# Kernel tuning notes

Measured on AMD Instinct MI355X. Metric: run time of the kernel, lower is better.

Reference implementation:

```python
import jax, jax.numpy as jnp
import numpy as np

B, S, D = 2, 2048, 1024
H = 16
DH = D // H  # 64


def setup_inputs() -> dict:
    key = jax.random.key(0)
    ks = jax.random.split(key, 5)
    scale = 0.02
    x = jax.random.normal(ks[0], (B, S, D), dtype=jnp.float32)
    W_qkv = jax.random.normal(ks[1], (D, 3 * D), dtype=jnp.float32) * scale
    b_qkv = jnp.zeros((3 * D,), dtype=jnp.float32)
    W_out = jax.random.normal(ks[2], (D, D), dtype=jnp.float32) * scale
    b_out = jnp.zeros((D,), dtype=jnp.float32)
    return {"x": x, "W_qkv": W_qkv, "b_qkv": b_qkv, "W_out": W_out, "b_out": b_out}


def reference(x, W_qkv, b_qkv, W_out, b_out):
    # Fused QKV projection: [B,S,D] @ [D,3D] -> [B,S,3D]
    qkv = jnp.einsum('bsd,df->bsf', x, W_qkv) + b_qkv
    q, k, v = qkv[:, :, :D], qkv[:, :, D:2 * D], qkv[:, :, 2 * D:]
    # Split heads: [B,S,D] -> [B,H,S,DH]
    def split(t):
        return t.reshape(B, S, H, DH).transpose(0, 2, 1, 3)
    q, k, v = split(q), split(k), split(v)
    # Scaled dot-product attention (naive, full score matrix as in source)
    scores = jnp.einsum('bhqd,bhkd->bhqk', q, k) / jnp.sqrt(jnp.float32(DH))
    probs = jax.nn.softmax(scores, axis=-1)  # mask=None, dropout eval-mode identity
    attn = jnp.einsum('bhqk,bhkd->bhqd', probs, v)
    # Merge heads: [B,H,S,DH] -> [B,S,D]
    attn = attn.transpose(0, 2, 1, 3).reshape(B, S, D)
    out = jnp.einsum('bsd,de->bse', attn, W_out) + b_out
    return out
```

## Files before the change

kernel.cpp:

```cpp
#include <hip/hip_runtime.h>

typedef _Float16 half8  __attribute__((ext_vector_type(8)));
typedef _Float16 half4  __attribute__((ext_vector_type(4)));
typedef float    floatx4  __attribute__((ext_vector_type(4)));
typedef float    floatx16 __attribute__((ext_vector_type(16)));

constexpr int B_ = 2, S_ = 2048, D_ = 1024, H_ = 16, M_ = 4096;
constexpr float QSCALE = 0.18033688011112042f;

__device__ __forceinline__ void gload16(const void* g, void* l) {
  __builtin_amdgcn_global_load_lds((const __attribute__((address_space(1))) void*)g,
                                   (__attribute__((address_space(3))) void*)l, 16, 0, 0);
}

__global__ __launch_bounds__(256) void cast_f32_f16(const float* __restrict__ in,
                                                    _Float16* __restrict__ out, int n8) {
  int i = blockIdx.x * 256 + threadIdx.x;
  if (i >= n8) return;
  float4 a = reinterpret_cast<const float4*>(in)[2 * i];
  float4 b = reinterpret_cast<const float4*>(in)[2 * i + 1];
  half8 h;
  h[0] = (_Float16)a.x; h[1] = (_Float16)a.y; h[2] = (_Float16)a.z; h[3] = (_Float16)a.w;
  h[4] = (_Float16)b.x; h[5] = (_Float16)b.y; h[6] = (_Float16)b.z; h[7] = (_Float16)b.w;
  reinterpret_cast<half8*>(out)[i] = h;
}

__global__ __launch_bounds__(256) void transpose_cast(const float* __restrict__ W,
                                                      _Float16* __restrict__ WT,
                                                      int K, int N) {
  __shared__ float Ws[64][65];
  const int n0 = blockIdx.x * 64, k0 = blockIdx.y * 64;
  const int t = threadIdx.x;
#pragma unroll
  for (int i = 0; i < 4; i++) {
    int idx = t + 256 * i;
    int r = idx >> 4, c4 = idx & 15;
    float4 v = *reinterpret_cast<const float4*>(W + (size_t)(k0 + r) * N + n0 + c4 * 4);
    Ws[r][c4 * 4 + 0] = v.x; Ws[r][c4 * 4 + 1] = v.y;
    Ws[r][c4 * 4 + 2] = v.z; Ws[r][c4 * 4 + 3] = v.w;
  }
  __syncthreads();
#pragma unroll
  for (int i = 0; i < 2; i++) {
    int idx = t + 256 * i;
    int r = idx >> 3, ck = idx & 7;
    half8 h;
#pragma unroll
    for (int j = 0; j < 8; j++) h[j] = (_Float16)Ws[ck * 8 + j][r];
    *reinterpret_cast<half8*>(WT + (size_t)(n0 + r) * K + k0 + ck * 8) = h;
  }
}

template <bool OUT_HALF>
__global__ __launch_bounds__(256) void gemm_mfma(const _Float16* __restrict__ A,
                                                 const _Float16* __restrict__ BT,
                                                 const float* __restrict__ bias,
                                                 void* __restrict__ Cout,
                                                 int M, int N, int K,
                                                 float scale_lo, int ncut) {
  __shared__ _Float16 As[128 * 64];
  __shared__ _Float16 Bs[128 * 64];
  const int t = threadIdx.x, w = t >> 6, lane = t & 63;
  const int m0 = blockIdx.y * 128, n0 = blockIdx.x * 128;
  const int wr = (w >> 1) * 64, wc = (w & 1) * 64;

  floatx4 acc[4][4] = {};

  for (int k0 = 0; k0 < K; k0 += 64) {
    __syncthreads();
#pragma unroll
    for (int i = 0; i < 4; i++) {
      int idx = t + 256 * i;
      int r = idx >> 3, c = idx & 7;
      int cs = c ^ (r & 7);
      gload16(A + (size_t)(m0 + r) * K + k0 + cs * 8, (char*)As + idx * 16);
      gload16(BT + (size_t)(n0 + r) * K + k0 + cs * 8, (char*)Bs + idx * 16);
    }
    __syncthreads();
#pragma unroll
    for (int ks = 0; ks < 2; ks++) {
      half8 af[4], bf[4];
#pragma unroll
      for (int r = 0; r < 4; r++) {
        int row = wr + r * 16 + (lane & 15);
        int ch = (ks * 4 + (lane >> 4)) ^ (row & 7);
        af[r] = *reinterpret_cast<const half8*>((const char*)As + row * 128 + ch * 16);
      }
#pragma unroll
      for (int c = 0; c < 4; c++) {
        int row = wc + c * 16 + (lane & 15);
        int ch = (ks * 4 + (lane >> 4)) ^ (row & 7);
        bf[c] = *reinterpret_cast<const half8*>((const char*)Bs + row * 128 + ch * 16);
      }
#pragma unroll
      for (int r = 0; r < 4; r++)
#pragma unroll
        for (int c = 0; c < 4; c++)
          acc[r][c] = __builtin_amdgcn_mfma_f32_16x16x32_f16(af[r], bf[c], acc[r][c], 0, 0, 0);
    }
  }

#pragma unroll
  for (int r = 0; r < 4; r++)
#pragma unroll
    for (int c = 0; c < 4; c++) {
      int col = n0 + wc + c * 16 + (lane & 15);
      float bv = bias[col];
      float sc = (col < ncut) ? scale_lo : 1.0f;
#pragma unroll
      for (int reg = 0; reg < 4; reg++) {
        int row = m0 + wr + r * 16 + (lane >> 4) * 4 + reg;
        float v = (acc[r][c][reg] + bv) * sc;
        if (OUT_HALF)
          reinterpret_cast<_Float16*>(Cout)[(size_t)row * N + col] = (_Float16)v;
        else
          reinterpret_cast<float*>(Cout)[(size_t)row * N + col] = v;
      }
    }
}

__global__ __launch_bounds__(256) void v_transpose(const _Float16* __restrict__ qkv,
                                                   _Float16* __restrict__ Vt) {
  __shared__ _Float16 Vs[64][72];
  const int s0 = blockIdx.x * 64, bh = blockIdx.y;
  const int b = bh >> 4, h = bh & 15;
  const int t = threadIdx.x;
#pragma unroll
  for (int i = 0; i < 2; i++) {
    int idx = t + 256 * i;
    int r = idx >> 3, c = idx & 7;
    half8 v = *reinterpret_cast<const half8*>(
        qkv + (size_t)(b * S_ + s0 + r) * (3 * D_) + 2 * D_ + h * 64 + c * 8);
    *reinterpret_cast<half8*>(&Vs[r][c * 8]) = v;
  }
  __syncthreads();
#pragma unroll
  for (int i = 0; i < 2; i++) {
    int idx = t + 256 * i;
    int d = idx >> 3, c = idx & 7;
    half8 o;
#pragma unroll
    for (int j = 0; j < 8; j++) o[j] = Vs[c * 8 + j][d];
    *reinterpret_cast<half8*>(Vt + ((size_t)bh * 64 + d) * S_ + s0 + c * 8) = o;
  }
}

__global__ __launch_bounds__(256) void flash_mfma(const _Float16* __restrict__ qkv,
                                                  const _Float16* __restrict__ Vt,
                                                  _Float16* __restrict__ attn_out) {
  const int qt = blockIdx.x, h = blockIdx.y, b = blockIdx.z;
  const int t = threadIdx.x, w = t >> 6, lane = t & 63;
  const int lo = lane & 31, hi = lane >> 5;

  __shared__ _Float16 Ks[64 * 64];
  __shared__ _Float16 Vts[64 * 64];
  __shared__ _Float16 Ps[4 * 2048];

  const int qrow = qt * 128 + w * 32 + lo;
  const _Float16* qbase = qkv + (size_t)(b * S_ + qrow) * (3 * D_) + h * 64;
  half8 qf[4];
#pragma unroll
  for (int kd = 0; kd < 4; kd++)
    qf[kd] = *reinterpret_cast<const half8*>(qbase + kd * 16 + hi * 8);

  floatx16 s0, s1, o0, o1;
#pragma unroll
  for (int r = 0; r < 16; r++) { o0[r] = 0.f; o1[r] = 0.f; }
  float m = -1e30f, l = 0.f;

  const size_t kbase = (size_t)(b * S_) * (3 * D_) + D_ + h * 64;
  const size_t vbase = (size_t)(b * H_ + h) * 64 * S_;

  for (int kv0 = 0; kv0 < S_; kv0 += 64) {
    __syncthreads();
#pragma unroll
    for (int i = 0; i < 2; i++) {
      int idx = t + 256 * i;
      int r = idx >> 3, c = idx & 7, cs = c ^ (r & 7);
      gload16(qkv + kbase + (size_t)(kv0 + r) * (3 * D_) + cs * 8, (char*)Ks + idx * 16);
      gload16(Vt + vbase + (size_t)r * S_ + kv0 + cs * 8, (char*)Vts + idx * 16);
    }
    __syncthreads();

#pragma unroll
    for (int r = 0; r < 16; r++) { s0[r] = 0.f; s1[r] = 0.f; }
#pragma unroll
    for (int kd = 0; kd < 4; kd++) {
      int r0 = lo, r1 = 32 + lo;
      int ch = kd * 2 + hi;
      half8 k0f = *reinterpret_cast<const half8*>((const char*)Ks + r0 * 128 + ((ch ^ (r0 & 7)) * 16));
      half8 k1f = *reinterpret_cast<const half8*>((const char*)Ks + r1 * 128 + ((ch ^ (r1 & 7)) * 16));
      s0 = __builtin_amdgcn_mfma_f32_32x32x16_f16(k0f, qf[kd], s0, 0, 0, 0);
      s1 = __builtin_amdgcn_mfma_f32_32x32x16_f16(k1f, qf[kd], s1, 0, 0, 0);
    }

    float pm = -1e30f;
#pragma unroll
    for (int r = 0; r < 16; r++) pm = fmaxf(pm, fmaxf(s0[r], s1[r]));
    pm = fmaxf(pm, __shfl_xor(pm, 32));
    float mn = fmaxf(m, pm);
    float alpha = __builtin_amdgcn_exp2f(m - mn);
    m = mn;
    float rs = 0.f;
#pragma unroll
    for (int r = 0; r < 16; r++) {
      s0[r] = __builtin_amdgcn_exp2f(s0[r] - mn);
      s1[r] = __builtin_amdgcn_exp2f(s1[r] - mn);
      rs += s0[r] + s1[r];
    }
    rs += __shfl_xor(rs, 32);
    l = l * alpha + rs;
#pragma unroll
    for (int r = 0; r < 16; r++) { o0[r] *= alpha; o1[r] *= alpha; }

#pragma unroll
    for (int mt = 0; mt < 2; mt++)
#pragma unroll
      for (int rq = 0; rq < 4; rq++) {
        half4 pv;
#pragma unroll
        for (int e = 0; e < 4; e++) pv[e] = (_Float16)((mt ? s1 : s0)[4 * rq + e]);
        int ch = (4 * mt + rq) ^ (lo & 7);
        *reinterpret_cast<half4*>((char*)Ps + w * 4096 + lo * 128 + ch * 16 + hi * 8) = pv;
      }

#pragma unroll
    for (int ks = 0; ks < 4; ks++) {
      int ch = ks * 2 + hi;
      half8 pf = *reinterpret_cast<const half8*>(
          (const char*)Ps + w * 4096 + lo * 128 + ((ch ^ (lo & 7)) * 16));
      int r0 = lo, r1 = 32 + lo;
      half8 vf0 = *reinterpret_cast<const half8*>((const char*)Vts + r0 * 128 + ((ch ^ (r0 & 7)) * 16));
      half8 vf1 = *reinterpret_cast<const half8*>((const char*)Vts + r1 * 128 + ((ch ^ (r1 & 7)) * 16));
      o0 = __builtin_amdgcn_mfma_f32_32x32x16_f16(vf0, pf, o0, 0, 0, 0);
      o1 = __builtin_amdgcn_mfma_f32_32x32x16_f16(vf1, pf, o1, 0, 0, 0);
    }
  }

  float inv = 1.0f / l;
  _Float16* ob = attn_out + (size_t)(b * S_ + qt * 128 + w * 32 + lo) * D_ + h * 64;
#pragma unroll
  for (int mt = 0; mt < 2; mt++)
#pragma unroll
    for (int rq = 0; rq < 4; rq++) {
      half4 v;
#pragma unroll
      for (int e = 0; e < 4; e++) v[e] = (_Float16)((mt ? o1 : o0)[4 * rq + e] * inv);
      *reinterpret_cast<half4*>(ob + 32 * mt + 8 * rq + 4 * hi) = v;
    }
}

extern "C" void kernel_launch(void* const* d_in, const int* in_sizes, int n_in,
                              void* d_out, int out_size, void* d_ws, size_t ws_size,
                              hipStream_t stream) {
  const float* x     = (const float*)d_in[0];
  const float* W_qkv = (const float*)d_in[1];
  const float* b_qkv = (const float*)d_in[2];
  const float* W_out = (const float*)d_in[3];
  const float* b_out = (const float*)d_in[4];
  float* out = (float*)d_out;

  _Float16* xh   = (_Float16*)d_ws;
  _Float16* WqT  = xh   + (size_t)M_ * D_;
  _Float16* WoT  = WqT  + (size_t)3 * D_ * D_;
  _Float16* qkvh = WoT  + (size_t)D_ * D_;
  _Float16* Vth  = qkvh + (size_t)M_ * 3 * D_;
  _Float16* atth = Vth  + (size_t)B_ * H_ * 64 * S_;

  cast_f32_f16<<<(M_ * D_ / 8 + 255) / 256, 256, 0, stream>>>(x, xh, M_ * D_ / 8);
  transpose_cast<<<dim3(3 * D_ / 64, D_ / 64), 256, 0, stream>>>(W_qkv, WqT, D_, 3 * D_);
  transpose_cast<<<dim3(D_ / 64, D_ / 64), 256, 0, stream>>>(W_out, WoT, D_, D_);

  gemm_mfma<true><<<dim3(3 * D_ / 128, M_ / 128), 256, 0, stream>>>(
      xh, WqT, b_qkv, qkvh, M_, 3 * D_, D_, QSCALE, D_);

  v_transpose<<<dim3(S_ / 64, B_ * H_), 256, 0, stream>>>(qkvh, Vth);

  flash_mfma<<<dim3(S_ / 128, H_, B_), 256, 0, stream>>>(qkvh, Vth, atth);

  gemm_mfma<false><<<dim3(D_ / 128, M_ / 128), 256, 0, stream>>>(
      atth, WoT, b_out, out, M_, D_, D_, 1.0f, 0);
}
```

Baseline: 151.5 us.

## Double-buffer 128-wide KV tiles and keep P in registers via permlane swap

Restructures the flash attention loop to process 128-key tiles with double-buffered K/V shared memory, prefetching the next tile with async global-to-LDS loads while the current one computes. The LDS round-trip for the probability matrix is removed: P is packed to fp16 in registers and rearranged with v_permlane32_swap to form the MFMA operand directly. It also adds a lazy rescale that skips the output rescaling when the running max grows by no more than a threshold. The costs are more LDS and register pressure, and one wasted prefetch of a wrapped tile on the last iteration.

```diff
diff --git a/kernel.cpp b/kernel.cpp
--- a/kernel.cpp
+++ b/kernel.cpp
@@ -4,9 +4,11 @@
 typedef _Float16 half4  __attribute__((ext_vector_type(4)));
 typedef float    floatx4  __attribute__((ext_vector_type(4)));
 typedef float    floatx16 __attribute__((ext_vector_type(16)));
+typedef unsigned int uint4v __attribute__((ext_vector_type(4)));
 
 constexpr int B_ = 2, S_ = 2048, D_ = 1024, H_ = 16, M_ = 4096;
 constexpr float QSCALE = 0.18033688011112042f;
+constexpr int KVB = 128, NTILES = S_ / KVB;
 
 __device__ __forceinline__ void gload16(const void* g, void* l) {
   __builtin_amdgcn_global_load_lds((const __attribute__((address_space(1))) void*)g,
@@ -152,9 +154,8 @@
   const int t = threadIdx.x, w = t >> 6, lane = t & 63;
   const int lo = lane & 31, hi = lane >> 5;
 
-  __shared__ _Float16 Ks[64 * 64];
-  __shared__ _Float16 Vts[64 * 64];
-  __shared__ _Float16 Ps[4 * 2048];
+  __shared__ _Float16 Ks[2][KVB * 64];
+  __shared__ _Float16 Vts[2][64 * KVB];
 
   const int qrow = qt * 128 + w * 32 + lo;
   const _Float16* qbase = qkv + (size_t)(b * S_ + qrow) * (3 * D_) + h * 64;
@@ -162,90 +163,120 @@
 #pragma unroll
   for (int kd = 0; kd < 4; kd++)
     qf[kd] = *reinterpret_cast<const half8*>(qbase + kd * 16 + hi * 8);
-
-  floatx16 s0, s1, o0, o1;
+  asm volatile("" : "+v"(qf[0]), "+v"(qf[1]), "+v"(qf[2]), "+v"(qf[3]));
+
+  const size_t kbase = (size_t)(b * S_) * (3 * D_) + D_ + h * 64;
+  const size_t vbase = (size_t)(b * H_ + h) * 64 * S_;
+
+  auto stage = [&](int buf, int tile) {
+    const int kv0 = tile * KVB;
+    const _Float16* kg = qkv + kbase + (size_t)kv0 * (3 * D_);
+#pragma unroll
+    for (int p = 0; p < 4; p++) {
+      int idx = t + 256 * p;
+      int r = idx >> 3, c = idx & 7, cs = c ^ (r & 7);
+      gload16(kg + (size_t)r * (3 * D_) + cs * 8, (char*)&Ks[buf][0] + idx * 16);
+    }
+    const _Float16* vg = Vt + vbase + kv0;
+#pragma unroll
+    for (int p = 0; p < 4; p++) {
+      int idx = t + 256 * p;
+      int r = idx >> 4, c = idx & 15, cs = c ^ (r & 15);
+      gload16(vg + (size_t)r * S_ + cs * 8, (char*)&Vts[buf][0] + idx * 16);
+    }
+  };
+
+  floatx16 o0, o1;
 #pragma unroll
   for (int r = 0; r < 16; r++) { o0[r] = 0.f; o1[r] = 0.f; }
   float m = -1e30f, l = 0.f;
 
-  const size_t kbase = (size_t)(b * S_) * (3 * D_) + D_ + h * 64;
-  const size_t vbase = (size_t)(b * H_ + h) * 64 * S_;
-
-  for (int kv0 = 0; kv0 < S_; kv0 += 64) {
-    __syncthreads();
-#pragma unroll
-    for (int i = 0; i < 2; i++) {
-      int idx = t + 256 * i;
-      int r = idx >> 3, c = idx & 7, cs = c ^ (r & 7);
-      gload16(qkv + kbase + (size_t)(kv0 + r) * (3 * D_) + cs * 8, (char*)Ks + idx * 16);
-      gload16(Vt + vbase + (size_t)r * S_ + kv0 + cs * 8, (char*)Vts + idx * 16);
-    }
-    __syncthreads();
-
-#pragma unroll
-    for (int r = 0; r < 16; r++) { s0[r] = 0.f; s1[r] = 0.f; }
+  stage(0, 0);
+
+  for (int tt = 0; tt < NTILES; ++tt) {
+    const int cb = tt & 1;
+    stage(cb ^ 1, (tt + 1) & (NTILES - 1));
+    asm volatile("s_waitcnt vmcnt(8)" ::: "memory");
+    __builtin_amdgcn_s_barrier();
+    __builtin_amdgcn_sched_barrier(0);
+
+    const char* kb2 = (const char*)&Ks[cb][0];
+    floatx16 s[4];
+#pragma unroll
+    for (int sb = 0; sb < 4; sb++)
+#pragma unroll
+      for (int r = 0; r < 16; r++) s[sb][r] = 0.f;
 #pragma unroll
     for (int kd = 0; kd < 4; kd++) {
-      int r0 = lo, r1 = 32 + lo;
-      int ch = kd * 2 + hi;
-      half8 k0f = *reinterpret_cast<const half8*>((const char*)Ks + r0 * 128 + ((ch ^ (r0 & 7)) * 16));
-      half8 k1f = *reinterpret_cast<const half8*>((const char*)Ks + r1 * 128 + ((ch ^ (r1 & 7)) * 16));
-      s0 = __builtin_amdgcn_mfma_f32_32x32x16_f16(k0f, qf[kd], s0, 0, 0, 0);
-      s1 = __builtin_amdgcn_mfma_f32_32x32x16_f16(k1f, qf[kd], s1, 0, 0, 0);
+#pragma unroll
+      for (int sb = 0; sb < 4; sb++) {
+        int rr = sb * 32 + lo;
+        half8 kf = *reinterpret_cast<const half8*>(
+            kb2 + rr * 128 + (((kd * 2 + hi) ^ (rr & 7)) * 16));
+        s[sb] = __builtin_amdgcn_mfma_f32_32x32x16_f16(kf, qf[kd], s[sb], 0, 0, 0);
+      }
     }
 
     float pm = -1e30f;
 #pragma unroll
-    for (int r = 0; r < 16; r++) pm = fmaxf(pm, fmaxf(s0[r], s1[r]));
+    for (int sb = 0; sb < 4; sb++)
+#pragma unroll
+      for (int r = 0; r < 16; r++) pm = fmaxf(pm, s[sb][r]);
     pm = fmaxf(pm, __shfl_xor(pm, 32));
-    float mn = fmaxf(m, pm);
-    float alpha = __builtin_amdgcn_exp2f(m - mn);
-    m = mn;
+    if (!__all(pm <= m + 8.0f)) {
+      float mn = fmaxf(m, pm);
+      float al = __builtin_amdgcn_exp2f(m - mn);
+      m = mn; l *= al;
+#pragma unroll
+      for (int r = 0; r < 16; r++) { o0[r] *= al; o1[r] *= al; }
+    }
     float rs = 0.f;
 #pragma unroll
-    for (int r = 0; r < 16; r++) {
-      s0[r] = __builtin_amdgcn_exp2f(s0[r] - mn);
-      s1[r] = __builtin_amdgcn_exp2f(s1[r] - mn);
-      rs += s0[r] + s1[r];
-    }
+    for (int sb = 0; sb < 4; sb++)
+#pragma unroll
+      for (int r = 0; r < 16; r++) {
+        s[sb][r] = __builtin_amdgcn_exp2f(s[sb][r] - m);
+        rs += s[sb][r];
+      }
     rs += __shfl_xor(rs, 32);
-    l = l * alpha + rs;
-#pragma unroll
-    for (int r = 0; r < 16; r++) { o0[r] *= alpha; o1[r] *= alpha; }
-
-#pragma unroll
-    for (int mt = 0; mt < 2; mt++)
-#pragma unroll
-      for (int rq = 0; rq < 4; rq++) {
-        half4 pv;
-#pragma unroll
-        for (int e = 0; e < 4; e++) pv[e] = (_Float16)((mt ? s1 : s0)[4 * rq + e]);
-        int ch = (4 * mt + rq) ^ (lo & 7);
-        *reinterpret_cast<half4*>((char*)Ps + w * 4096 + lo * 128 + ch * 16 + hi * 8) = pv;
-      }
-
-#pragma unroll
-    for (int ks = 0; ks < 4; ks++) {
-      int ch = ks * 2 + hi;
-      half8 pf = *reinterpret_cast<const half8*>(
-          (const char*)Ps + w * 4096 + lo * 128 + ((ch ^ (lo & 7)) * 16));
-      int r0 = lo, r1 = 32 + lo;
-      half8 vf0 = *reinterpret_cast<const half8*>((const char*)Vts + r0 * 128 + ((ch ^ (r0 & 7)) * 16));
-      half8 vf1 = *reinterpret_cast<const half8*>((const char*)Vts + r1 * 128 + ((ch ^ (r1 & 7)) * 16));
-      o0 = __builtin_amdgcn_mfma_f32_32x32x16_f16(vf0, pf, o0, 0, 0, 0);
-      o1 = __builtin_amdgcn_mfma_f32_32x32x16_f16(vf1, pf, o1, 0, 0, 0);
-    }
+    l += rs;
+
+    const char* vb2 = (const char*)&Vts[cb][0];
+#pragma unroll
+    for (int sb = 0; sb < 4; sb++) {
+#pragma unroll
+      for (int hf = 0; hf < 2; hf++) {
+        const int rb = hf * 8;
+        unsigned w0a = __builtin_bit_cast(unsigned, __builtin_amdgcn_cvt_pkrtz(s[sb][rb + 0], s[sb][rb + 1]));
+        unsigned w0b = __builtin_bit_cast(unsigned, __builtin_amdgcn_cvt_pkrtz(s[sb][rb + 4], s[sb][rb + 5]));
+        unsigned w1a = __builtin_bit_cast(unsigned, __builtin_amdgcn_cvt_pkrtz(s[sb][rb + 2], s[sb][rb + 3]));
+        unsigned w1b = __builtin_bit_cast(unsigned, __builtin_amdgcn_cvt_pkrtz(s[sb][rb + 6], s[sb][rb + 7]));
+        asm("v_permlane32_swap_b32 %0, %1" : "+v"(w0a), "+v"(w0b));
+        asm("v_permlane32_swap_b32 %0, %1" : "+v"(w1a), "+v"(w1b));
+        uint4v u; u[0] = w0a; u[1] = w1a; u[2] = w0b; u[3] = w1b;
+        half8 pf = __builtin_bit_cast(half8, u);
+        const int ks = sb * 2 + hf;
+        const int ch = ks * 2 + hi;
+        half8 vf0 = *reinterpret_cast<const half8*>(vb2 + lo * 256 + ((ch ^ (lo & 15)) * 16));
+        half8 vf1 = *reinterpret_cast<const half8*>(vb2 + (lo + 32) * 256 + ((ch ^ (lo & 15)) * 16));
+        o0 = __builtin_amdgcn_mfma_f32_32x32x16_f16(vf0, pf, o0, 0, 0, 0);
+        o1 = __builtin_amdgcn_mfma_f32_32x32x16_f16(vf1, pf, o1, 0, 0, 0);
+      }
+    }
+
+    __builtin_amdgcn_sched_barrier(0);
+    __builtin_amdgcn_s_barrier();
   }
 
   float inv = 1.0f / l;
-  _Float16* ob = attn_out + (size_t)(b * S_ + qt * 128 + w * 32 + lo) * D_ + h * 64;
+  _Float16* ob = attn_out + (size_t)(b * S_ + qrow) * D_ + h * 64;
 #pragma unroll
   for (int mt = 0; mt < 2; mt++)
 #pragma unroll
     for (int rq = 0; rq < 4; rq++) {
       half4 v;
 #pragma unroll
-      for (int e = 0; e < 4; e++) v[e] = (_Float16)((mt ? o1 : o0)[4 * rq + e] * inv);
+      for (int e = 0; e < 4; e++) v[e] = (_Float16)(((mt ? o1 : o0)[4 * rq + e]) * inv);
       *reinterpret_cast<half4*>(ob + 32 * mt + 8 * rq + 4 * hi) = v;
     }
 }
```

Measured after the change: 154.8 us. 2.2% more time.
